# Kernel tuning notes

Hardware: AMD Instinct MI355X
Metric: run time of the kernel (lower is better)

Reference implementation:

```python
import jax, jax.numpy as jnp
import numpy as np

EPS = 1e-5

def _conv1x1(x, W, b):
    # x: [B,Ci,H,W], W: [Co,Ci]
    return jnp.einsum('oi,bihw->bohw', W, x) + b[None, :, None, None]

def _bn(x, gamma, beta, mean, var):
    # inference-mode BatchNorm2d
    s = gamma / jnp.sqrt(var + EPS)
    return x * s[None, :, None, None] + (beta - mean * s)[None, :, None, None]

def _conv3x3(x, W, b):
    y = jax.lax.conv_general_dilated(x, W, (1, 1), 'SAME',
                                     dimension_numbers=('NCHW', 'OIHW', 'NCHW'))
    return y + b[None, :, None, None]

def _sparsemax_last(S):
    # sparsemax over the last axis (TrackHSPA: max-subtract, sort, cumsum, threshold)
    S = S - jnp.max(S, axis=-1, keepdims=True)
    srt = -jnp.sort(-S, axis=-1)                 # descending sort
    csum = jnp.cumsum(srt, axis=-1) - 1.0
    N = S.shape[-1]
    ar = jnp.arange(1, N + 1, dtype=S.dtype)
    mask = ar * srt > csum
    k = jnp.sum(mask, axis=-1, keepdims=True)    # support size per row
    tau = jnp.take_along_axis(csum, k - 1, axis=-1) / k.astype(S.dtype)
    return jnp.maximum(S - tau, 0.0)

def _forward(zf, xf, Wq, bq, Ws, bs, Wg, bg, g_gamma, g_beta, g_mean, g_var,
             Wfi, bfi, fi_gamma, fi_beta, fi_mean, fi_var,
             Wm, bm, m_gamma, m_beta, m_mean, m_var, prelu_a):
    B, C, Hx, Wx = xf.shape
    # ---- Graph_Attention_Union (cross-attention) ----
    xf_t = _conv1x1(xf, Wq, bq).reshape(B, C, -1)      # [B,C,Nx]
    zf_t = _conv1x1(zf, Ws, bs).reshape(B, C, -1)      # [B,C,Nz]
    xf_g = jax.nn.relu(_bn(_conv1x1(xf, Wg, bg), g_gamma, g_beta, g_mean, g_var))
    zf_g = jax.nn.relu(_bn(_conv1x1(zf, Wg, bg), g_gamma, g_beta, g_mean, g_var))
    sim = jnp.einsum('bcn,bcm->bnm', xf_t, zf_t)       # [B,Nx,Nz]
    attn = jax.nn.softmax(sim, axis=2)
    emb = jnp.einsum('bcm,bnm->bcn', zf_g.reshape(B, C, -1), attn)
    emb = emb.reshape(B, C, Hx, Wx)
    gat = jax.nn.relu(_bn(_conv1x1(jnp.concatenate([emb, xf_g], axis=1), Wfi, bfi),
                          fi_gamma, fi_beta, fi_mean, fi_var))
    # ---- TrackHSPA (adaptive sparsemax self-attention) ----
    e = _conv3x3(gat, Wm, bm)
    e = _bn(e, m_gamma, m_beta, m_mean, m_var)
    e = jnp.where(e >= 0, e, prelu_a * e)              # PReLU (single param)
    N = Hx * Wx
    ef = e.reshape(B, -1, N)                           # [B,C',N]
    S = jnp.einsum('bdi,bdj->bij', ef, ef)             # [B,N,N]
    P = _sparsemax_last(S)
    out = jnp.einsum('bcn,bnm->bcm', gat.reshape(B, C, N), P)
    return out.reshape(B, C, Hx, Wx) + gat


def setup_inputs():
    key = jax.random.key(0)
    ks = jax.random.split(key, 8)
    B, C, Hz, Wz, Hx, Wx = 32, 256, 7, 7, 31, 31
    Cm = C // 4
    f = lambda k, shape: jax.random.normal(k, shape, jnp.float32) * 0.05
    return {
        'zf': jax.random.normal(ks[0], (B, C, Hz, Wz), jnp.float32),
        'xf': jax.random.normal(ks[1], (B, C, Hx, Wx), jnp.float32),
        'Wq': f(ks[2], (C, C)), 'bq': jnp.zeros((C,), jnp.float32),
        'Ws': f(ks[3], (C, C)), 'bs': jnp.zeros((C,), jnp.float32),
        'Wg': f(ks[4], (C, C)), 'bg': jnp.zeros((C,), jnp.float32),
        'g_gamma': jnp.ones((C,), jnp.float32), 'g_beta': jnp.zeros((C,), jnp.float32),
        'g_mean': jnp.zeros((C,), jnp.float32), 'g_var': jnp.ones((C,), jnp.float32),
        'Wfi': f(ks[5], (C, 2 * C)), 'bfi': jnp.zeros((C,), jnp.float32),
        'fi_gamma': jnp.ones((C,), jnp.float32), 'fi_beta': jnp.zeros((C,), jnp.float32),
        'fi_mean': jnp.zeros((C,), jnp.float32), 'fi_var': jnp.ones((C,), jnp.float32),
        'Wm': f(ks[6], (Cm, C, 3, 3)), 'bm': jnp.zeros((Cm,), jnp.float32),
        'm_gamma': jnp.ones((Cm,), jnp.float32), 'm_beta': jnp.zeros((Cm,), jnp.float32),
        'm_mean': jnp.zeros((Cm,), jnp.float32), 'm_var': jnp.ones((Cm,), jnp.float32),
        'prelu_a': jnp.array(0.25, jnp.float32),
    }


def reference(zf, xf, Wq, bq, Ws, bs, Wg, bg, g_gamma, g_beta, g_mean, g_var,
              Wfi, bfi, fi_gamma, fi_beta, fi_mean, fi_var,
              Wm, bm, m_gamma, m_beta, m_mean, m_var, prelu_a):
    return _forward(zf, xf, Wq, bq, Ws, bs, Wg, bg, g_gamma, g_beta, g_mean, g_var,
                    Wfi, bfi, fi_gamma, fi_beta, fi_mean, fi_var,
                    Wm, bm, m_gamma, m_beta, m_mean, m_var, prelu_a)
```

## Files before the change

### kernel.cpp

```cpp
#include <hip/hip_runtime.h>
#include <cstdint>
#include <cstddef>
#include <math.h>

typedef __attribute__((ext_vector_type(8))) short short8;
typedef __attribute__((ext_vector_type(4))) float floatx4;
typedef unsigned short ushort_t;

__device__ __forceinline__ ushort_t f2bf(float x) {
    union { float f; unsigned u; } v; v.f = x;
    unsigned r = v.u + 0x7FFF + ((v.u >> 16) & 1);
    return (ushort_t)(r >> 16);
}
__device__ __forceinline__ float bf2f(ushort_t h) {
    union { unsigned u; float f; } v; v.u = ((unsigned)h) << 16; return v.f;
}
__device__ __forceinline__ void split2(float v, ushort_t& h, ushort_t& l) {
    h = f2bf(v);
    l = f2bf(v - bf2f(h));
}

#define MFMA(a, b, c) __builtin_amdgcn_mfma_f32_16x16x32_bf16((a), (b), (c), 0, 0, 0)

__device__ __forceinline__ void gload_lds16(const void* g, void* l) {
    __builtin_amdgcn_global_load_lds(
        (const __attribute__((address_space(1))) unsigned*)g,
        (__attribute__((address_space(3))) unsigned*)l, 16, 0, 0);
}

__global__ void prep_all_kernel(
    const float* __restrict__ Wq, const float* __restrict__ Ws,
    const float* __restrict__ Wg, const float* __restrict__ Wfi,
    const float* __restrict__ Wm,
    const float* bq, const float* bs,
    const float* bg, const float* gg, const float* gb, const float* gm, const float* gv,
    const float* bfi, const float* fg, const float* fb, const float* fm, const float* fv,
    const float* bm, const float* mg, const float* mb, const float* mm, const float* mv,
    ushort_t* Wq_h, ushort_t* Wq_l, ushort_t* Ws_h, ushort_t* Ws_l,
    ushort_t* Wg_h, ushort_t* Wg_l, ushort_t* Wfi_h, ushort_t* Wfi_l,
    ushort_t* wm_h, ushort_t* wm_l, float* scsh)
{
    int bid = blockIdx.x, t = threadIdx.x;
    if (bid < 256) {
        int i = bid * 256 + t; ushort_t h, l; split2(Wq[i], h, l); Wq_h[i] = h; Wq_l[i] = l;
    } else if (bid < 512) {
        int i = (bid - 256) * 256 + t; ushort_t h, l; split2(Ws[i], h, l); Ws_h[i] = h; Ws_l[i] = l;
    } else if (bid < 768) {
        int i = (bid - 512) * 256 + t; ushort_t h, l; split2(Wg[i], h, l); Wg_h[i] = h; Wg_l[i] = l;
    } else if (bid < 1280) {
        int i = (bid - 768) * 256 + t; ushort_t h, l; split2(Wfi[i], h, l); Wfi_h[i] = h; Wfi_l[i] = l;
    } else if (bid < 1856) {
        int i = (bid - 1280) * 256 + t;
        int c = i & 255, m = (i >> 8) & 63, tap = i >> 14;
        ushort_t h, l; split2(Wm[((size_t)m * 256 + c) * 9 + tap], h, l);
        wm_h[i] = h; wm_l[i] = l;
    } else {
        if (t < 256) {
            scsh[t] = 1.f;        scsh[256 + t] = bq[t];
            scsh[512 + t] = 1.f;  scsh[768 + t] = bs[t];
            float s = gg[t] * rsqrtf(gv[t] + 1e-5f);
            scsh[1024 + t] = s;   scsh[1280 + t] = gb[t] + s * (bg[t] - gm[t]);
            float s2 = fg[t] * rsqrtf(fv[t] + 1e-5f);
            scsh[1536 + t] = s2;  scsh[1792 + t] = fb[t] + s2 * (bfi[t] - fm[t]);
            if (t < 64) {
                float s3 = mg[t] * rsqrtf(mv[t] + 1e-5f);
                scsh[2048 + t] = s3; scsh[2112 + t] = mb[t] + s3 * (bm[t] - mm[t]);
            }
        }
    }
}

__global__ void halo_zero_kernel(ushort_t* __restrict__ gxh, ushort_t* __restrict__ gxl) {
    int i = blockIdx.x * 256 + threadIdx.x;
    int b = i >> 7, k = i & 127;
    int r;
    if (k < 33) r = k;
    else if (k < 66) r = 32 * 33 + (k - 33);
    else { int k2 = k - 66; r = ((k2 >> 1) + 1) * 33 + ((k2 & 1) ? 32 : 0); }
    uint4* ph = (uint4*)(gxh + ((size_t)b * 1089 + r) * 256);
    uint4* pl = (uint4*)(gxl + ((size_t)b * 1089 + r) * 256);
    uint4 z = make_uint4(0, 0, 0, 0);
#pragma unroll
    for (int s = 0; s < 32; s++) { ph[s] = z; pl[s] = z; }
}

__global__ __launch_bounds__(256) void transpose_in_kernel(
    const float* __restrict__ in, ushort_t* __restrict__ oh, ushort_t* __restrict__ ol,
    int Nsrc, int Npad)
{
    int b = blockIdx.z;
    const float* ib = in + (size_t)b * 256 * Nsrc;
    ushort_t* obh = oh + (size_t)b * Npad * 256;
    ushort_t* obl = ol + (size_t)b * Npad * 256;
    __shared__ float tile[32][33];
    int n0 = blockIdx.x * 32, c0 = blockIdx.y * 32;
    int tx = threadIdx.x & 31, ty = threadIdx.x >> 5;
#pragma unroll
    for (int r = 0; r < 4; r++) {
        int c = c0 + ty + r * 8, n = n0 + tx;
        tile[ty + r * 8][tx] = (n < Nsrc) ? ib[(size_t)c * Nsrc + n] : 0.f;
    }
    __syncthreads();
#pragma unroll
    for (int r = 0; r < 4; r++) {
        int n = n0 + ty + r * 8, c = c0 + tx;
        if (n < Nsrc) {
            ushort_t h, l; split2(tile[tx][ty + r * 8], h, l);
            obh[(size_t)n * 256 + c] = h;
            obl[(size_t)n * 256 + c] = l;
        }
    }
}

__global__ __launch_bounds__(256, 2) void dualconv_mfma_kernel(
    const ushort_t* __restrict__ Xh, const ushort_t* __restrict__ Xl,
    const ushort_t* __restrict__ W1h, const ushort_t* __restrict__ W1l,
    const ushort_t* __restrict__ W2h, const ushort_t* __restrict__ W2l,
    const float* __restrict__ sc1, const float* __restrict__ sh1,
    const float* __restrict__ sc2, const float* __restrict__ sh2,
    int relu1, int relu2,
    ushort_t* __restrict__ O1h, ushort_t* __restrict__ O1l,
    ushort_t* __restrict__ O2h, ushort_t* __restrict__ O2l,
    ushort_t* __restrict__ O2ch, ushort_t* __restrict__ O2cl, int cpitch,
    int K, int Nvalid, int NpadIn, int NpadOut)
{
    __shared__ ushort_t Bs[32768];
    int b = blockIdx.x;
    int n0 = blockIdx.y * 64;
    const ushort_t* Xbh = Xh + (size_t)b * NpadIn * K;
    const ushort_t* Xbl = Xl + (size_t)b * NpadIn * K;
    int tid = threadIdx.x, w = tid >> 6, l = tid & 63, lc = l & 15, q = l >> 4;
    int m0 = w * 64;

#pragma unroll
    for (int r = 0; r < 16; r++) {
        int d = r * 4096 + w * 1024 + l * 16;
        int dr = d & 32767;
        int row = dr >> 9;
        int inrow = (dr & 511) ^ ((row & 7) << 4);
        int srow = n0 + row; if (srow > NpadIn - 1) srow = NpadIn - 1;
        const ushort_t* src = ((d >> 15) ? Xbl : Xbh) + (size_t)srow * K + (inrow >> 1);
        char* dst = (char*)Bs + (r * 4096 + w * 1024);
        gload_lds16(src, dst);
    }
    __syncthreads();

#define DC_LOADA(K0, AH, AL) do { \
    _Pragma("unroll") \
    for (int mt_ = 0; mt_ < 4; mt_++) { \
        size_t off_ = (size_t)(m0 + mt_ * 16 + lc) * K + (K0) + q * 8; \
        AH[mt_] = *(const short8*)(Wh + off_); \
        AL[mt_] = *(const short8*)(Wl + off_); \
    } \
} while (0)
#define DC_LDSB(K0, BH, BL) do { \
    _Pragma("unroll") \
    for (int jt_ = 0; jt_ < 4; jt_++) { \
        int row_ = jt_ * 16 + lc; \
        int koff_ = (((K0) + q * 8) * 2) ^ ((row_ & 7) << 4); \
        BH[jt_] = *(const short8*)((const char*)Bs + row_ * 512 + koff_); \
        BL[jt_] = *(const short8*)((const char*)Bs + 32768 + row_ * 512 + koff_); \
    } \
} while (0)
#define DC_MFMA(AH, AL, BH, BL) do { \
    _Pragma("unroll") \
    for (int mt_ = 0; mt_ < 4; mt_++) \
    _Pragma("unroll") \
    for (int jt_ = 0; jt_ < 4; jt_++) { \
        acc[mt_][jt_] = MFMA(AH[mt_], BH[jt_], acc[mt_][jt_]); \
        acc[mt_][jt_] = MFMA(AH[mt_], BL[jt_], acc[mt_][jt_]); \
        acc[mt_][jt_] = MFMA(AL[mt_], BH[jt_], acc[mt_][jt_]); \
    } \
} while (0)

    for (int half = 0; half < 2; half++) {
        const ushort_t* Wh = half ? W2h : W1h;
        const ushort_t* Wl = half ? W2l : W1l;
        const float* sc = half ? sc2 : sc1;
        const float* sh = half ? sh2 : sh1;
        int relu = half ? relu2 : relu1;
        ushort_t* Obh = (half ? O2h : O1h) + (size_t)b * NpadOut * 256;
        ushort_t* Obl = (half ? O2l : O1l) + (size_t)b * NpadOut * 256;

        floatx4 acc[4][4];
#pragma unroll
        for (int i = 0; i < 4; i++)
#pragma unroll
            for (int j = 0; j < 4; j++) acc[i][j] = (floatx4){0.f, 0.f, 0.f, 0.f};

        short8 ah0[4], al0[4], ah1[4], al1[4], bh[4], bl[4];
        DC_LOADA(0, ah0, al0);
        for (int k0 = 0; k0 < K; k0 += 64) {
            DC_LOADA(k0 + 32, ah1, al1);
            DC_LDSB(k0, bh, bl);
            DC_MFMA(ah0, al0, bh, bl);
            if (k0 + 64 < K) DC_LOADA(k0 + 64, ah0, al0);
            DC_LDSB(k0 + 32, bh, bl);
            DC_MFMA(ah1, al1, bh, bl);
        }

#pragma unroll
        for (int mt = 0; mt < 4; mt++) {
            int mb = m0 + mt * 16 + q * 4;
            float s0 = sc[mb], s1 = sc[mb + 1], s2 = sc[mb + 2], s3 = sc[mb + 3];
            float h0 = sh[mb], h1 = sh[mb + 1], h2 = sh[mb + 2], h3 = sh[mb + 3];
#pragma unroll
            for (int jt = 0; jt < 4; jt++) {
                int n = n0 + jt * 16 + lc;
                if (n >= Nvalid) continue;
                float v0 = acc[mt][jt][0] * s0 + h0;
                float v1 = acc[mt][jt][1] * s1 + h1;
                float v2 = acc[mt][jt][2] * s2 + h2;
                float v3 = acc[mt][jt][3] * s3 + h3;
                if (relu) { v0 = fmaxf(v0, 0.f); v1 = fmaxf(v1, 0.f); v2 = fmaxf(v2, 0.f); v3 = fmaxf(v3, 0.f); }
                ushort_t e0, f0, e1, f1, e2, f2, e3, f3;
                split2(v0, e0, f0); split2(v1, e1, f1); split2(v2, e2, f2); split2(v3, e3, f3);
                *(ushort4*)(Obh + (size_t)n * 256 + mb) = make_ushort4(e0, e1, e2, e3);
                *(ushort4*)(Obl + (size_t)n * 256 + mb) = make_ushort4(f0, f1, f2, f3);
                if (half && O2ch) {
                    O2ch[((size_t)b * 256 + mb + 0) * cpitch + n] = e0;
                    O2ch[((size_t)b * 256 + mb + 1) * cpitch + n] = e1;
                    O2ch[((size_t)b * 256 + mb + 2) * cpitch + n] = e2;
                    O2ch[((size_t)b * 256 + mb + 3) * cpitch + n] = e3;
                    O2cl[((size_t)b * 256 + mb + 0) * cpitch + n] = f0;
                    O2cl[((size_t)b * 256 + mb + 1) * cpitch + n] = f1;
                    O2cl[((size_t)b * 256 + mb + 2) * cpitch + n] = f2;
                    O2cl[((size_t)b * 256 + mb + 3) * cpitch + n] = f3;
                }
            }
        }
    }
#undef DC_LOADA
#undef DC_LDSB
#undef DC_MFMA
}

__global__ __launch_bounds__(256) void attn_mfma_kernel(
    const ushort_t* __restrict__ xth, const ushort_t* __restrict__ xtl,
    const ushort_t* __restrict__ zth, const ushort_t* __restrict__ ztl,
    const ushort_t* __restrict__ zgh, const ushort_t* __restrict__ zgl,
    ushort_t* __restrict__ eh, ushort_t* __restrict__ el)
{
    __shared__ float S[64][68];
    __shared__ ushort_t awh[64][72], awl[64][72];
    __shared__ float T[4][16][20];
    int b = blockIdx.x, n0 = blockIdx.y * 64;
    int tid = threadIdx.x, w = tid >> 6, l = tid & 63, lc = l & 15, q = l >> 4;
    const ushort_t* xhb = xth + (size_t)b * 992 * 256;
    const ushort_t* xlb = xtl + (size_t)b * 992 * 256;
    const ushort_t* zhb = zth + (size_t)b * 64 * 256;
    const ushort_t* zlb = ztl + (size_t)b * 64 * 256;
    const ushort_t* ghb = zgh + (size_t)b * 256 * 64;
    const ushort_t* glb = zgl + (size_t)b * 256 * 64;

    int rowg = n0 + w * 16 + lc;
#pragma unroll
    for (int ct = 0; ct < 4; ct++) {
        floatx4 acc = (floatx4){0.f, 0.f, 0.f, 0.f};
        for (int k0 = 0; k0 < 256; k0 += 32) {
            short8 ah = *(const short8*)(xhb + (size_t)rowg * 256 + k0 + q * 8);
            short8 al = *(const short8*)(xlb + (size_t)rowg * 256 + k0 + q * 8);
            short8 bh = *(const short8*)(zhb + (size_t)(ct * 16 + lc) * 256 + k0 + q * 8);
            short8 bl = *(const short8*)(zlb + (size_t)(ct * 16 + lc) * 256 + k0 + q * 8);
            acc = MFMA(ah, bh, acc);
            acc = MFMA(ah, bl, acc);
            acc = MFMA(al, bh, acc);
        }
#pragma unroll
        for (int r = 0; r < 4; r++) S[w * 16 + q * 4 + r][ct * 16 + lc] = acc[r];
    }
    __syncthreads();
    if (tid < 64) {
        float mx = -INFINITY;
        for (int m = 0; m < 49; m++) mx = fmaxf(mx, S[tid][m]);
        float sum = 0.f;
        for (int m = 0; m < 49; m++) { float e = __expf(S[tid][m] - mx); S[tid][m] = e; sum += e; }
        float inv = 1.f / sum;
        for (int m = 0; m < 64; m++) {
            float vv = (m < 49) ? S[tid][m] * inv : 0.f;
            ushort_t hh, ll; split2(vv, hh, ll);
            awh[tid][m] = hh; awl[tid][m] = ll;
        }
    }
    __syncthreads();
    int nw = l >> 2, cg = l & 3;
#pragma unroll
    for (int ct = 0; ct < 16; ct++) {
        floatx4 acc = (floatx4){0.f, 0.f, 0.f, 0.f};
#pragma unroll
        for (int k0 = 0; k0 < 64; k0 += 32) {
            short8 ah = *(const short8*)(&awh[w * 16 + lc][k0 + q * 8]);
            short8 al = *(const short8*)(&awl[w * 16 + lc][k0 + q * 8]);
            short8 bh = *(const short8*)(ghb + (size_t)(ct * 16 + lc) * 64 + k0 + q * 8);
            short8 bl = *(const short8*)(glb + (size_t)(ct * 16 + lc) * 64 + k0 + q * 8);
            acc = MFMA(ah, bh, acc);
            acc = MFMA(ah, bl, acc);
            acc = MFMA(al, bh, acc);
        }
#pragma unroll
        for (int r = 0; r < 4; r++) T[w][q * 4 + r][lc] = acc[r];
        float4 vv = *(const float4*)&T[w][nw][cg * 4];
        int n = n0 + w * 16 + nw;
        if (n < 961) {
            ushort_t h0, l0, h1, l1, h2, l2_, h3, l3;
            split2(vv.x, h0, l0); split2(vv.y, h1, l1);
            split2(vv.z, h2, l2_); split2(vv.w, h3, l3);
            size_t off = ((size_t)b * 992 + n) * 256 + ct * 16 + cg * 4;
            *(ushort4*)(eh + off) = make_ushort4(h0, h1, h2, h3);
            *(ushort4*)(el + off) = make_ushort4(l0, l1, l2_, l3);
        }
    }
}

__global__ __launch_bounds__(256, 2) void fi_mfma_kernel(
    const ushort_t* __restrict__ Eh, const ushort_t* __restrict__ El,
    const ushort_t* __restrict__ Gh, const ushort_t* __restrict__ Gl,
    const ushort_t* __restrict__ Wh, const ushort_t* __restrict__ Wl,
    const float* __restrict__ sc, const float* __restrict__ sh,
    ushort_t* __restrict__ gxh, ushort_t* __restrict__ gxl,
    ushort_t* __restrict__ gat_nf)
{
    __shared__ ushort_t Bs[32768];
    int b = blockIdx.x;
    const ushort_t* Ebh = Eh + (size_t)b * 992 * 256;
    const ushort_t* Ebl = El + (size_t)b * 992 * 256;
    const ushort_t* Gbh = Gh + (size_t)b * 992 * 256;
    const ushort_t* Gbl = Gl + (size_t)b * 992 * 256;
    ushort_t* gxhb = gxh + (size_t)b * 1089 * 256;
    ushort_t* gxlb = gxl + (size_t)b * 1089 * 256;
    ushort_t* gn = gat_nf + (size_t)b * 256 * 992;
    int tid = threadIdx.x, w = tid >> 6, l = tid & 63, lc = l & 15, q = l >> 4;
    int m0 = w * 64, nb0 = blockIdx.y * 32;

#pragma unroll
    for (int r = 0; r < 16; r++) {
        int d = r * 4096 + w * 1024 + l * 16;
        int seg = d >> 14;
        int dr = d & 16383;
        int row = dr >> 9;
        int inrow = (dr & 511) ^ ((row & 7) << 4);
        int srow = nb0 + row; if (srow > 991) srow = 991;
        const ushort_t* base = (seg == 0) ? Ebh : (seg == 1) ? Ebl : (seg == 2) ? Gbh : Gbl;
        const ushort_t* src = base + (size_t)srow * 256 + (inrow >> 1);
        char* dst = (char*)Bs + (r * 4096 + w * 1024);
        gload_lds16(src, dst);
    }
    __syncthreads();

    floatx4 acc[4][2];
#pragma unroll
    for (int i = 0; i < 4; i++)
#pragma unroll
        for (int j = 0; j < 2; j++) acc[i][j] = (floatx4){0.f, 0.f, 0.f, 0.f};

#define FI_LOADA(K0, AH, AL) do { \
    _Pragma("unroll") \
    for (int mt_ = 0; mt_ < 4; mt_++) { \
        size_t off_ = (size_t)(m0 + mt_ * 16 + lc) * 512 + (K0) + q * 8; \
        AH[mt_] = *(const short8*)(Wh + off_); \
        AL[mt_] = *(const short8*)(Wl + off_); \
    } \
} while (0)
#define FI_LDSB(K0, BH, BL) do { \
    int segb_ = ((K0) < 256) ? 0 : 32768; \
    int kk_ = (K0) & 255; \
    _Pragma("unroll") \
    for (int jt_ = 0; jt_ < 2; jt_++) { \
        int row_ = jt_ * 16 + lc; \
        int koff_ = ((kk_ + q * 8) * 2) ^ ((row_ & 7) << 4); \
        BH[jt_] = *(const short8*)((const char*)Bs + segb_ + row_ * 512 + koff_); \
        BL[jt_] = *(const short8*)((const char*)Bs + segb_ + 16384 + row_ * 512 + koff_); \
    } \
} while (0)
#define FI_MFMA(AH, AL, BH, BL) do { \
    _Pragma("unroll") \
    for (int mt_ = 0; mt_ < 4; mt_++) \
    _Pragma("unroll") \
    for (int jt_ = 0; jt_ < 2; jt_++) { \
        acc[mt_][jt_] = MFMA(AH[mt_], BH[jt_], acc[mt_][jt_]); \
        acc[mt_][jt_] = MFMA(AH[mt_], BL[jt_], acc[mt_][jt_]); \
        acc[mt_][jt_] = MFMA(AL[mt_], BH[jt_], acc[mt_][jt_]); \
    } \
} while (0)

    {
        short8 ah0[4], al0[4], ah1[4], al1[4], bh[2], bl[2];
        FI_LOADA(0, ah0, al0);
        for (int k0 = 0; k0 < 512; k0 += 64) {
            FI_LOADA(k0 + 32, ah1, al1);
            FI_LDSB(k0, bh, bl);
            FI_MFMA(ah0, al0, bh, bl);
            if (k0 + 64 < 512) FI_LOADA(k0 + 64, ah0, al0);
            FI_LDSB(k0 + 32, bh, bl);
            FI_MFMA(ah1, al1, bh, bl);
        }
    }
#undef FI_LOADA
#undef FI_LDSB
#undef FI_MFMA

#pragma unroll
    for (int mt = 0; mt < 4; mt++) {
        int mb = m0 + mt * 16 + q * 4;
        float s0 = sc[mb], s1 = sc[mb + 1], s2 = sc[mb + 2], s3 = sc[mb + 3];
        float h0 = sh[mb], h1 = sh[mb + 1], h2 = sh[mb + 2], h3 = sh[mb + 3];
#pragma unroll
        for (int jt = 0; jt < 2; jt++) {
            int n = nb0 + jt * 16 + lc;
            if (n >= 961) continue;
            float v0 = fmaxf(acc[mt][jt][0] * s0 + h0, 0.f);
            float v1 = fmaxf(acc[mt][jt][1] * s1 + h1, 0.f);
            float v2 = fmaxf(acc[mt][jt][2] * s2 + h2, 0.f);
            float v3 = fmaxf(acc[mt][jt][3] * s3 + h3, 0.f);
            ushort_t a0, b0, a1, b1, a2, b2, a3, b3;
            split2(v0, a0, b0); split2(v1, a1, b1); split2(v2, a2, b2); split2(v3, a3, b3);
            int hh = n / 31, ww2 = n - hh * 31;
            int row = (hh + 1) * 33 + (ww2 + 1);
            *(ushort4*)(gxhb + (size_t)row * 256 + mb) = make_ushort4(a0, a1, a2, a3);
            *(ushort4*)(gxlb + (size_t)row * 256 + mb) = make_ushort4(b0, b1, b2, b3);
            gn[(size_t)(mb + 0) * 992 + n] = a0;
            gn[(size_t)(mb + 1) * 992 + n] = a1;
            gn[(size_t)(mb + 2) * 992 + n] = a2;
            gn[(size_t)(mb + 3) * 992 + n] = a3;
        }
    }
}

__global__ __launch_bounds__(256, 2) void conv3x3_mfma_kernel(
    const ushort_t* __restrict__ gxh, const ushort_t* __restrict__ gxl,
    const ushort_t* __restrict__ wmh, const ushort_t* __restrict__ wml,
    const float* __restrict__ sc, const float* __restrict__ sh,
    const float* __restrict__ prelu_a,
    ushort_t* __restrict__ eh, ushort_t* __restrict__ el)
{
    __shared__ float Sp[4][2048];
    int b = blockIdx.x;
    const ushort_t* gxhb = gxh + (size_t)b * 1089 * 256;
    const ushort_t* gxlb = gxl + (size_t)b * 1089 * 256;
    ushort_t* ebh = eh + (size_t)b * 1024 * 64;
    ushort_t* ebl = el + (size_t)b * 1024 * 64;
    int tid = threadIdx.x, w = tid >> 6, l = tid & 63, lc = l & 15, q = l >> 4;
    int j0 = blockIdx.y * 64;

    int base[4];
#pragma unroll
    for (int jt = 0; jt < 4; jt++) {
        int j = j0 + jt * 16 + lc; if (j > 960) j = 960;
        int hh = j / 31, ww2 = j - hh * 31;
        base[jt] = (hh + 1) * 33 + (ww2 + 1);
    }

    floatx4 acc[4][4];
#pragma unroll
    for (int i = 0; i < 4; i++)
#pragma unroll
        for (int j = 0; j < 4; j++) acc[i][j] = (floatx4){0.f, 0.f, 0.f, 0.f};

#define C3_LOAD(SL, AH, AL, BH, BL) do { \
    int sl_ = (SL); \
    int tap_ = (sl_ >= 9) ? sl_ - 9 : sl_; \
    int k0_ = (w * 2 + ((sl_ >= 9) ? 1 : 0)) * 32; \
    int doff_ = (tap_ / 3 - 1) * 33 + (tap_ % 3 - 1); \
    const ushort_t* wth_ = wmh + tap_ * 16384; \
    const ushort_t* wtl_ = wml + tap_ * 16384; \
    _Pragma("unroll") \
    for (int mt_ = 0; mt_ < 4; mt_++) { \
        size_t off_ = (size_t)(mt_ * 16 + lc) * 256 + k0_ + q * 8; \
        AH[mt_] = *(const short8*)(wth_ + off_); \
        AL[mt_] = *(const short8*)(wtl_ + off_); \
    } \
    _Pragma("unroll") \
    for (int jt_ = 0; jt_ < 4; jt_++) { \
        size_t off_ = (size_t)(base[jt_] + doff_) * 256 + k0_ + q * 8; \
        BH[jt_] = *(const short8*)(gxhb + off_); \
        BL[jt_] = *(const short8*)(gxlb + off_); \
    } \
} while (0)
#define C3_MFMA(AH, AL, BH, BL) do { \
    _Pragma("unroll") \
    for (int mt_ = 0; mt_ < 4; mt_++) \
    _Pragma("unroll") \
    for (int jt_ = 0; jt_ < 4; jt_++) { \
        acc[mt_][jt_] = MFMA(AH[mt_], BH[jt_], acc[mt_][jt_]); \
        acc[mt_][jt_] = MFMA(AH[mt_], BL[jt_], acc[mt_][jt_]); \
        acc[mt_][jt_] = MFMA(AL[mt_], BH[jt_], acc[mt_][jt_]); \
    } \
} while (0)

    short8 A0h[4], A0l[4], B0h[4], B0l[4];
    short8 A1h[4], A1l[4], B1h[4], B1l[4];
    C3_LOAD(0, A0h, A0l, B0h, B0l);
#pragma unroll
    for (int it = 0; it < 9; it++) {
        C3_LOAD(it * 2 + 1, A1h, A1l, B1h, B1l);
        C3_MFMA(A0h, A0l, B0h, B0l);
        if (it < 8) C3_LOAD(it * 2 + 2, A0h, A0l, B0h, B0l);
        C3_MFMA(A1h, A1l, B1h, B1l);
    }
#undef C3_LOAD
#undef C3_MFMA

    float pa = prelu_a[0];
#pragma unroll
    for (int ph = 0; ph < 2; ph++) {
        __syncthreads();
#pragma unroll
        for (int mt = 0; mt < 4; mt++)
#pragma unroll
            for (int jt = 0; jt < 2; jt++)
#pragma unroll
                for (int r = 0; r < 4; r++)
                    Sp[w][(mt * 16 + q * 4 + r) * 32 + jt * 16 + lc] = acc[mt][ph * 2 + jt][r];
        __syncthreads();
#pragma unroll
        for (int gi = 0; gi < 2; gi++) {
            int g = tid + gi * 256;
            int j = g & 31, mg = g >> 5;
            int m = mg * 4;
            int jj = j0 + ph * 32 + j;
            if (jj >= 961) continue;
            float v[4];
#pragma unroll
            for (int i = 0; i < 4; i++) {
                int idx = (m + i) * 32 + j;
                v[i] = Sp[0][idx] + Sp[1][idx] + Sp[2][idx] + Sp[3][idx];
                v[i] = v[i] * sc[m + i] + sh[m + i];
                v[i] = v[i] >= 0.f ? v[i] : pa * v[i];
            }
            ushort_t a0, b0, a1, b1, a2, b2, a3, b3;
            split2(v[0], a0, b0); split2(v[1], a1, b1);
            split2(v[2], a2, b2); split2(v[3], a3, b3);
            *(ushort4*)(ebh + (size_t)jj * 64 + m) = make_ushort4(a0, a1, a2, a3);
            *(ushort4*)(ebl + (size_t)jj * 64 + m) = make_ushort4(b0, b1, b2, b3);
        }
    }
}

__global__ __launch_bounds__(512) void hspa_mfma_kernel(
    const ushort_t* __restrict__ eh, const ushort_t* __restrict__ el,
    ushort_t* __restrict__ PT)
{
    const int PITCH = 978;
    __shared__ float S[16 * 978];
    int b = blockIdx.x, nb = blockIdx.y;
    const ushort_t* ebh = eh + (size_t)b * 1024 * 64;
    const ushort_t* ebl = el + (size_t)b * 1024 * 64;
    ushort_t* Pb = PT + (size_t)b * 1024 * 992;
    int tid = threadIdx.x, w = tid >> 6, l = tid & 63, lc = l & 15, q = l >> 4;
    int n0 = nb * 16;

    short8 a0h = *(const short8*)(ebh + (size_t)(n0 + lc) * 64 + q * 8);
    short8 a0l = *(const short8*)(ebl + (size_t)(n0 + lc) * 64 + q * 8);
    short8 a1h = *(const short8*)(ebh + (size_t)(n0 + lc) * 64 + 32 + q * 8);
    short8 a1l = *(const short8*)(ebl + (size_t)(n0 + lc) * 64 + 32 + q * 8);

    for (int jt = w; jt < 61; jt += 8) {
        int j = jt * 16 + lc;
        short8 b0h = *(const short8*)(ebh + (size_t)j * 64 + q * 8);
        short8 b0l = *(const short8*)(ebl + (size_t)j * 64 + q * 8);
        short8 b1h = *(const short8*)(ebh + (size_t)j * 64 + 32 + q * 8);
        short8 b1l = *(const short8*)(ebl + (size_t)j * 64 + 32 + q * 8);
        floatx4 acc = (floatx4){0.f, 0.f, 0.f, 0.f};
        acc = MFMA(a0h, b0h, acc);
        acc = MFMA(a0h, b0l, acc);
        acc = MFMA(a0l, b0h, acc);
        acc = MFMA(a1h, b1h, acc);
        acc = MFMA(a1h, b1l, acc);
        acc = MFMA(a1l, b1h, acc);
#pragma unroll
        for (int r = 0; r < 4; r++) S[(q * 4 + r) * PITCH + j] = acc[r];
    }
    __syncthreads();

    int r0 = w * 2, r1 = w * 2 + 1;
    float sv0[16], sv1[16];
    float mx0 = -INFINITY, mx1 = -INFINITY;
#pragma unroll
    for (int t = 0; t < 16; t++) {
        int j = l + t * 64;
        float s0 = (j < 961) ? S[r0 * PITCH + j] : -INFINITY;
        float s1 = (j < 961) ? S[r1 * PITCH + j] : -INFINITY;
        sv0[t] = s0; sv1[t] = s1;
        mx0 = fmaxf(mx0, s0); mx1 = fmaxf(mx1, s1);
    }
    for (int off = 32; off; off >>= 1) {
        mx0 = fmaxf(mx0, __shfl_xor(mx0, off));
        mx1 = fmaxf(mx1, __shfl_xor(mx1, off));
    }
#pragma unroll
    for (int t = 0; t < 16; t++) { sv0[t] -= mx0; sv1[t] -= mx1; }

    float tau0 = -1.f, tau1 = -1.f;
    for (int it = 0; it < 16; it++) {
        float s0 = 0.f, c0 = 0.f, s1 = 0.f, c1 = 0.f;
#pragma unroll
        for (int t = 0; t < 16; t++) {
            if (sv0[t] > tau0) { s0 += sv0[t]; c0 += 1.f; }
            if (sv1[t] > tau1) { s1 += sv1[t]; c1 += 1.f; }
        }
        for (int off = 32; off; off >>= 1) {
            s0 += __shfl_xor(s0, off); c0 += __shfl_xor(c0, off);
            s1 += __shfl_xor(s1, off); c1 += __shfl_xor(c1, off);
        }
        float nt0 = (s0 - 1.f) / c0;
        float nt1 = (s1 - 1.f) / c1;
        bool conv = (nt0 == tau0) && (nt1 == tau1);
        tau0 = nt0; tau1 = nt1;
        if (conv) break;
    }
#pragma unroll
    for (int t = 0; t < 16; t++) {
        int j = l + t * 64;
        if (j < 976) {
            S[r0 * PITCH + j] = (j < 961) ? fmaxf(sv0[t] - tau0, 0.f) : 0.f;
            S[r1 * PITCH + j] = (j < 961) ? fmaxf(sv1[t] - tau1, 0.f) : 0.f;
        }
    }
    __syncthreads();

    for (int j = tid; j < 976; j += 512) {
        union { ushort_t u[8]; uint4 v; } p0, p1;
#pragma unroll
        for (int r = 0; r < 8; r++)  p0.u[r] = f2bf(S[r * PITCH + j]);
#pragma unroll
        for (int r = 0; r < 8; r++)  p1.u[r] = f2bf(S[(8 + r) * PITCH + j]);
        ushort_t* dst = Pb + (size_t)j * 992 + n0;
        *(uint4*)(dst) = p0.v;
        *(uint4*)(dst + 8) = p1.v;
    }
}

__global__ __launch_bounds__(256, 2) void out_mfma_kernel(
    const ushort_t* __restrict__ gat_nf, const ushort_t* __restrict__ PT,
    float* __restrict__ out)
{
    int b = blockIdx.x, jb = blockIdx.y;
    const ushort_t* gb = gat_nf + (size_t)b * 256 * 992;
    const ushort_t* Pb = PT + (size_t)b * 1024 * 992;
    float* ob = out + (size_t)b * 256 * 961;
    int tid = threadIdx.x, w = tid >> 6, l = tid & 63, lc = l & 15, q = l >> 4;
    int m0 = w * 64, j0 = jb * 64;

    floatx4 acc[4][4];
#pragma unroll
    for (int i = 0; i < 4; i++)
#pragma unroll
        for (int j = 0; j < 4; j++) acc[i][j] = (floatx4){0.f, 0.f, 0.f, 0.f};

#define OUT_LOAD(K0, AA, BB) do { \
    _Pragma("unroll") \
    for (int mt_ = 0; mt_ < 4; mt_++) \
        AA[mt_] = *(const short8*)(gb + (size_t)(m0 + mt_ * 16 + lc) * 992 + (K0) + q * 8); \
    _Pragma("unroll") \
    for (int jt_ = 0; jt_ < 4; jt_++) \
        BB[jt_] = *(const short8*)(Pb + (size_t)(j0 + jt_ * 16 + lc) * 992 + (K0) + q * 8); \
} while (0)
#define OUT_MFMA(AA, BB) do { \
    _Pragma("unroll") \
    for (int mt_ = 0; mt_ < 4; mt_++) \
    _Pragma("unroll") \
    for (int jt_ = 0; jt_ < 4; jt_++) \
        acc[mt_][jt_] = MFMA(AA[mt_], BB[jt_], acc[mt_][jt_]); \
} while (0)

    short8 a0[4], b0[4], a1[4], b1[4];
    OUT_LOAD(0, a0, b0);
    for (int k0 = 0; k0 < 960; k0 += 64) {
        OUT_LOAD(k0 + 32, a1, b1);
        OUT_MFMA(a0, b0);
        OUT_LOAD(k0 + 64, a0, b0);
        OUT_MFMA(a1, b1);
    }
    OUT_MFMA(a0, b0);
#undef OUT_LOAD
#undef OUT_MFMA

#pragma unroll
    for (int mt = 0; mt < 4; mt++) {
        int mb = m0 + mt * 16 + q * 4;
#pragma unroll
        for (int jt = 0; jt < 4; jt++) {
            int j = j0 + jt * 16 + lc;
            if (j >= 961) continue;
#pragma unroll
            for (int r = 0; r < 4; r++) {
                float g = bf2f(gb[(size_t)(mb + r) * 992 + j]);
                ob[(size_t)(mb + r) * 961 + j] = acc[mt][jt][r] + g;
            }
        }
    }
}

extern "C" void kernel_launch(void* const* d_in, const int* in_sizes, int n_in,
                              void* d_out, int out_size, void* d_ws, size_t ws_size,
                              hipStream_t stream)
{
    const float* zf      = (const float*)d_in[0];
    const float* xf      = (const float*)d_in[1];
    const float* Wq      = (const float*)d_in[2];
    const float* bq      = (const float*)d_in[3];
    const float* Ws      = (const float*)d_in[4];
    const float* bs      = (const float*)d_in[5];
    const float* Wg      = (const float*)d_in[6];
    const float* bg      = (const float*)d_in[7];
    const float* g_gamma = (const float*)d_in[8];
    const float* g_beta  = (const float*)d_in[9];
    const float* g_mean  = (const float*)d_in[10];
    const float* g_var   = (const float*)d_in[11];
    const float* Wfi     = (const float*)d_in[12];
    const float* bfi     = (const float*)d_in[13];
    const float* fi_gamma= (const float*)d_in[14];
    const float* fi_beta = (const float*)d_in[15];
    const float* fi_mean = (const float*)d_in[16];
    const float* fi_var  = (const float*)d_in[17];
    const float* Wm      = (const float*)d_in[18];
    const float* bm      = (const float*)d_in[19];
    const float* m_gamma = (const float*)d_in[20];
    const float* m_beta  = (const float*)d_in[21];
    const float* m_mean  = (const float*)d_in[22];
    const float* m_var   = (const float*)d_in[23];
    const float* prelu_a = (const float*)d_in[24];
    float* out = (float*)d_out;

    ushort_t* ws = (ushort_t*)d_ws;
    ushort_t* Wq_h  = ws + 0;         ushort_t* Wq_l  = ws + 65536;
    ushort_t* Ws_h  = ws + 131072;    ushort_t* Ws_l  = ws + 196608;
    ushort_t* Wg_h  = ws + 262144;    ushort_t* Wg_l  = ws + 327680;
    ushort_t* Wfi_h = ws + 393216;    ushort_t* Wfi_l = ws + 524288;
    ushort_t* wm_h  = ws + 655360;    ushort_t* wm_l  = ws + 802816;
    ushort_t* XT_h    = ws + 950272;
    ushort_t* XT_l    = ws + 9076736;
    ushort_t* xf_tT_h = ws + 17203200;
    ushort_t* xf_tT_l = ws + 25329664;
    ushort_t* zf_tT_h = ws + 33456128;
    ushort_t* zf_tT_l = ws + 33980416;
    ushort_t* zf_gT_h = ws + 34504704;
    ushort_t* zf_gT_l = ws + 35028992;
    ushort_t* gxT_h   = ws + 17203200;
    ushort_t* gxT_l   = ws + 26124288;
    ushort_t* xf_gT_h = ws + 35553280;
    ushort_t* xf_gT_l = ws + 43679744;
    ushort_t* gat_nf  = ws + 51806208;
    ushort_t* eT_h    = ws + 59932672;
    ushort_t* eT_l    = ws + 62029824;
    ushort_t* PT      = ws + 64126976;
    ushort_t* zfT_h   = ws + 96632832;
    ushort_t* zfT_l   = ws + 97157120;
    float* scsh       = (float*)(ws + 97681408);
    ushort_t* zgC_h   = ws + 97685760;
    ushort_t* zgC_l   = ws + 98210048;
    ushort_t* embT_h = XT_h;
    ushort_t* embT_l = XT_l;

    const float* sc_q  = scsh + 0,    *sh_q  = scsh + 256;
    const float* sc_s  = scsh + 512,  *sh_s  = scsh + 768;
    const float* sc_g  = scsh + 1024, *sh_g  = scsh + 1280;
    const float* sc_fi = scsh + 1536, *sh_fi = scsh + 1792;
    const float* sc_m  = scsh + 2048, *sh_m  = scsh + 2112;

    prep_all_kernel<<<1857, 256, 0, stream>>>(
        Wq, Ws, Wg, Wfi, Wm,
        bq, bs, bg, g_gamma, g_beta, g_mean, g_var,
        bfi, fi_gamma, fi_beta, fi_mean, fi_var,
        bm, m_gamma, m_beta, m_mean, m_var,
        Wq_h, Wq_l, Ws_h, Ws_l, Wg_h, Wg_l, Wfi_h, Wfi_l, wm_h, wm_l, scsh);

    transpose_in_kernel<<<dim3(31, 8, 32), 256, 0, stream>>>(xf, XT_h, XT_l, 961, 992);
    transpose_in_kernel<<<dim3(2, 8, 32), 256, 0, stream>>>(zf, zfT_h, zfT_l, 49, 64);

    dualconv_mfma_kernel<<<dim3(32, 16), 256, 0, stream>>>(
        XT_h, XT_l, Wq_h, Wq_l, Wg_h, Wg_l,
        sc_q, sh_q, sc_g, sh_g, 0, 1,
        xf_tT_h, xf_tT_l, xf_gT_h, xf_gT_l,
        nullptr, nullptr, 0, 256, 961, 992, 992);
    dualconv_mfma_kernel<<<dim3(32, 1), 256, 0, stream>>>(
        zfT_h, zfT_l, Ws_h, Ws_l, Wg_h, Wg_l,
        sc_s, sh_s, sc_g, sh_g, 0, 1,
        zf_tT_h, zf_tT_l, zf_gT_h, zf_gT_l,
        zgC_h, zgC_l, 64, 256, 49, 64, 64);

    attn_mfma_kernel<<<dim3(32, 16), 256, 0, stream>>>(
        xf_tT_h, xf_tT_l, zf_tT_h, zf_tT_l, zgC_h, zgC_l, embT_h, embT_l);

    halo_zero_kernel<<<16, 256, 0, stream>>>(gxT_h, gxT_l);

    fi_mfma_kernel<<<dim3(32, 31), 256, 0, stream>>>(
        embT_h, embT_l, xf_gT_h, xf_gT_l, Wfi_h, Wfi_l, sc_fi, sh_fi,
        gxT_h, gxT_l, gat_nf);

    conv3x3_mfma_kernel<<<dim3(32, 16), 256, 0, stream>>>(
        gxT_h, gxT_l, wm_h, wm_l, sc_m, sh_m, prelu_a, eT_h, eT_l);

    hspa_mfma_kernel<<<dim3(32, 61), 512, 0, stream>>>(eT_h, eT_l, PT);

    out_mfma_kernel<<<dim3(32, 16), 256, 0, stream>>>(gat_nf, PT, out);
}
```

Before: 580.5 us.

## Halve tile sizes and LDS use in dualconv, fi and hspa kernels

Shrinks the dualconv tile from 64 to 32 columns with half the shared memory, and doubles its grid. The fi kernel now stages the E and G operands through one half-size LDS buffer in two passes instead of loading both at once. The hspa kernel processes 8 rows per block instead of 16, with half the shared memory and twice the blocks. The goal is more resident blocks and more parallelism, at the cost of extra A-operand reloads, an added barrier in fi, and idle lanes in hspa, where half the MFMA output rows are discarded.

```diff
diff --git a/kernel.cpp b/kernel.cpp
--- a/kernel.cpp
+++ b/kernel.cpp
@@ -124,22 +124,23 @@
     ushort_t* __restrict__ O2ch, ushort_t* __restrict__ O2cl, int cpitch,
     int K, int Nvalid, int NpadIn, int NpadOut)
 {
-    __shared__ ushort_t Bs[32768];
+    __shared__ ushort_t Bs[16384];
     int b = blockIdx.x;
-    int n0 = blockIdx.y * 64;
+    int n0 = blockIdx.y * 32;
     const ushort_t* Xbh = Xh + (size_t)b * NpadIn * K;
     const ushort_t* Xbl = Xl + (size_t)b * NpadIn * K;
     int tid = threadIdx.x, w = tid >> 6, l = tid & 63, lc = l & 15, q = l >> 4;
     int m0 = w * 64;
 
 #pragma unroll
-    for (int r = 0; r < 16; r++) {
+    for (int r = 0; r < 8; r++) {
         int d = r * 4096 + w * 1024 + l * 16;
-        int dr = d & 32767;
+        int seg = d >> 14;
+        int dr = d & 16383;
         int row = dr >> 9;
         int inrow = (dr & 511) ^ ((row & 7) << 4);
         int srow = n0 + row; if (srow > NpadIn - 1) srow = NpadIn - 1;
-        const ushort_t* src = ((d >> 15) ? Xbl : Xbh) + (size_t)srow * K + (inrow >> 1);
+        const ushort_t* src = (seg ? Xbl : Xbh) + (size_t)srow * K + (inrow >> 1);
         char* dst = (char*)Bs + (r * 4096 + w * 1024);
         gload_lds16(src, dst);
     }
@@ -155,18 +156,18 @@
 } while (0)
 #define DC_LDSB(K0, BH, BL) do { \
     _Pragma("unroll") \
-    for (int jt_ = 0; jt_ < 4; jt_++) { \
+    for (int jt_ = 0; jt_ < 2; jt_++) { \
         int row_ = jt_ * 16 + lc; \
         int koff_ = (((K0) + q * 8) * 2) ^ ((row_ & 7) << 4); \
         BH[jt_] = *(const short8*)((const char*)Bs + row_ * 512 + koff_); \
-        BL[jt_] = *(const short8*)((const char*)Bs + 32768 + row_ * 512 + koff_); \
+        BL[jt_] = *(const short8*)((const char*)Bs + 16384 + row_ * 512 + koff_); \
     } \
 } while (0)
 #define DC_MFMA(AH, AL, BH, BL) do { \
     _Pragma("unroll") \
     for (int mt_ = 0; mt_ < 4; mt_++) \
     _Pragma("unroll") \
-    for (int jt_ = 0; jt_ < 4; jt_++) { \
+    for (int jt_ = 0; jt_ < 2; jt_++) { \
         acc[mt_][jt_] = MFMA(AH[mt_], BH[jt_], acc[mt_][jt_]); \
         acc[mt_][jt_] = MFMA(AH[mt_], BL[jt_], acc[mt_][jt_]); \
         acc[mt_][jt_] = MFMA(AL[mt_], BH[jt_], acc[mt_][jt_]); \
@@ -182,13 +183,13 @@
         ushort_t* Obh = (half ? O2h : O1h) + (size_t)b * NpadOut * 256;
         ushort_t* Obl = (half ? O2l : O1l) + (size_t)b * NpadOut * 256;
 
-        floatx4 acc[4][4];
+        floatx4 acc[4][2];
 #pragma unroll
         for (int i = 0; i < 4; i++)
 #pragma unroll
-            for (int j = 0; j < 4; j++) acc[i][j] = (floatx4){0.f, 0.f, 0.f, 0.f};
-
-        short8 ah0[4], al0[4], ah1[4], al1[4], bh[4], bl[4];
+            for (int j = 0; j < 2; j++) acc[i][j] = (floatx4){0.f, 0.f, 0.f, 0.f};
+
+        short8 ah0[4], al0[4], ah1[4], al1[4], bh[2], bl[2];
         DC_LOADA(0, ah0, al0);
         for (int k0 = 0; k0 < K; k0 += 64) {
             DC_LOADA(k0 + 32, ah1, al1);
@@ -205,7 +206,7 @@
             float s0 = sc[mb], s1 = sc[mb + 1], s2 = sc[mb + 2], s3 = sc[mb + 3];
             float h0 = sh[mb], h1 = sh[mb + 1], h2 = sh[mb + 2], h3 = sh[mb + 3];
 #pragma unroll
-            for (int jt = 0; jt < 4; jt++) {
+            for (int jt = 0; jt < 2; jt++) {
                 int n = n0 + jt * 16 + lc;
                 if (n >= Nvalid) continue;
                 float v0 = acc[mt][jt][0] * s0 + h0;
@@ -320,7 +321,7 @@
     ushort_t* __restrict__ gxh, ushort_t* __restrict__ gxl,
     ushort_t* __restrict__ gat_nf)
 {
-    __shared__ ushort_t Bs[32768];
+    __shared__ ushort_t Bs[16384];
     int b = blockIdx.x;
     const ushort_t* Ebh = Eh + (size_t)b * 992 * 256;
     const ushort_t* Ebl = El + (size_t)b * 992 * 256;
@@ -332,21 +333,6 @@
     int tid = threadIdx.x, w = tid >> 6, l = tid & 63, lc = l & 15, q = l >> 4;
     int m0 = w * 64, nb0 = blockIdx.y * 32;
 
-#pragma unroll
-    for (int r = 0; r < 16; r++) {
-        int d = r * 4096 + w * 1024 + l * 16;
-        int seg = d >> 14;
-        int dr = d & 16383;
-        int row = dr >> 9;
-        int inrow = (dr & 511) ^ ((row & 7) << 4);
-        int srow = nb0 + row; if (srow > 991) srow = 991;
-        const ushort_t* base = (seg == 0) ? Ebh : (seg == 1) ? Ebl : (seg == 2) ? Gbh : Gbl;
-        const ushort_t* src = base + (size_t)srow * 256 + (inrow >> 1);
-        char* dst = (char*)Bs + (r * 4096 + w * 1024);
-        gload_lds16(src, dst);
-    }
-    __syncthreads();
-
     floatx4 acc[4][2];
 #pragma unroll
     for (int i = 0; i < 4; i++)
@@ -362,14 +348,12 @@
     } \
 } while (0)
 #define FI_LDSB(K0, BH, BL) do { \
-    int segb_ = ((K0) < 256) ? 0 : 32768; \
-    int kk_ = (K0) & 255; \
     _Pragma("unroll") \
     for (int jt_ = 0; jt_ < 2; jt_++) { \
         int row_ = jt_ * 16 + lc; \
-        int koff_ = ((kk_ + q * 8) * 2) ^ ((row_ & 7) << 4); \
-        BH[jt_] = *(const short8*)((const char*)Bs + segb_ + row_ * 512 + koff_); \
-        BL[jt_] = *(const short8*)((const char*)Bs + segb_ + 16384 + row_ * 512 + koff_); \
+        int koff_ = (((K0) + q * 8) * 2) ^ ((row_ & 7) << 4); \
+        BH[jt_] = *(const short8*)((const char*)Bs + row_ * 512 + koff_); \
+        BL[jt_] = *(const short8*)((const char*)Bs + 16384 + row_ * 512 + koff_); \
     } \
 } while (0)
 #define FI_MFMA(AH, AL, BH, BL) do { \
@@ -383,15 +367,33 @@
     } \
 } while (0)
 
-    {
+    for (int p = 0; p < 2; p++) {
+        const ushort_t* srcH = p ? Gbh : Ebh;
+        const ushort_t* srcL = p ? Gbl : Ebl;
+        if (p) __syncthreads();
+#pragma unroll
+        for (int r = 0; r < 8; r++) {
+            int d = r * 4096 + w * 1024 + l * 16;
+            int seg = d >> 14;
+            int dr = d & 16383;
+            int row = dr >> 9;
+            int inrow = (dr & 511) ^ ((row & 7) << 4);
+            int srow = nb0 + row; if (srow > 991) srow = 991;
+            const ushort_t* src = (seg ? srcL : srcH) + (size_t)srow * 256 + (inrow >> 1);
+            char* dst = (char*)Bs + (r * 4096 + w * 1024);
+            gload_lds16(src, dst);
+        }
+        __syncthreads();
+
+        int pb = p * 256;
         short8 ah0[4], al0[4], ah1[4], al1[4], bh[2], bl[2];
-        FI_LOADA(0, ah0, al0);
-        for (int k0 = 0; k0 < 512; k0 += 64) {
-            FI_LOADA(k0 + 32, ah1, al1);
-            FI_LDSB(k0, bh, bl);
+        FI_LOADA(pb, ah0, al0);
+        for (int kk = 0; kk < 256; kk += 64) {
+            FI_LOADA(pb + kk + 32, ah1, al1);
+            FI_LDSB(kk, bh, bl);
             FI_MFMA(ah0, al0, bh, bl);
-            if (k0 + 64 < 512) FI_LOADA(k0 + 64, ah0, al0);
-            FI_LDSB(k0 + 32, bh, bl);
+            if (kk + 64 < 256) FI_LOADA(pb + kk + 64, ah0, al0);
+            FI_LDSB(kk + 32, bh, bl);
             FI_MFMA(ah1, al1, bh, bl);
         }
     }
@@ -541,13 +543,13 @@
     ushort_t* __restrict__ PT)
 {
     const int PITCH = 978;
-    __shared__ float S[16 * 978];
+    __shared__ float S[8 * 978];
     int b = blockIdx.x, nb = blockIdx.y;
     const ushort_t* ebh = eh + (size_t)b * 1024 * 64;
     const ushort_t* ebl = el + (size_t)b * 1024 * 64;
     ushort_t* Pb = PT + (size_t)b * 1024 * 992;
     int tid = threadIdx.x, w = tid >> 6, l = tid & 63, lc = l & 15, q = l >> 4;
-    int n0 = nb * 16;
+    int n0 = nb * 8;
 
     short8 a0h = *(const short8*)(ebh + (size_t)(n0 + lc) * 64 + q * 8);
     short8 a0l = *(const short8*)(ebl + (size_t)(n0 + lc) * 64 + q * 8);
@@ -567,66 +569,55 @@
         acc = MFMA(a1h, b1h, acc);
         acc = MFMA(a1h, b1l, acc);
         acc = MFMA(a1l, b1h, acc);
-#pragma unroll
-        for (int r = 0; r < 4; r++) S[(q * 4 + r) * PITCH + j] = acc[r];
+        if (q < 2) {
+#pragma unroll
+            for (int r = 0; r < 4; r++) S[(q * 4 + r) * PITCH + j] = acc[r];
+        }
     }
     __syncthreads();
 
-    int r0 = w * 2, r1 = w * 2 + 1;
-    float sv0[16], sv1[16];
-    float mx0 = -INFINITY, mx1 = -INFINITY;
+    int r0 = w;
+    float sv0[16];
+    float mx0 = -INFINITY;
 #pragma unroll
     for (int t = 0; t < 16; t++) {
         int j = l + t * 64;
         float s0 = (j < 961) ? S[r0 * PITCH + j] : -INFINITY;
-        float s1 = (j < 961) ? S[r1 * PITCH + j] : -INFINITY;
-        sv0[t] = s0; sv1[t] = s1;
-        mx0 = fmaxf(mx0, s0); mx1 = fmaxf(mx1, s1);
-    }
-    for (int off = 32; off; off >>= 1) {
-        mx0 = fmaxf(mx0, __shfl_xor(mx0, off));
-        mx1 = fmaxf(mx1, __shfl_xor(mx1, off));
-    }
-#pragma unroll
-    for (int t = 0; t < 16; t++) { sv0[t] -= mx0; sv1[t] -= mx1; }
-
-    float tau0 = -1.f, tau1 = -1.f;
+        sv0[t] = s0;
+        mx0 = fmaxf(mx0, s0);
+    }
+    for (int off = 32; off; off >>= 1) mx0 = fmaxf(mx0, __shfl_xor(mx0, off));
+#pragma unroll
+    for (int t = 0; t < 16; t++) sv0[t] -= mx0;
+
+    float tau0 = -1.f;
     for (int it = 0; it < 16; it++) {
-        float s0 = 0.f, c0 = 0.f, s1 = 0.f, c1 = 0.f;
+        float s0 = 0.f, c0 = 0.f;
 #pragma unroll
         for (int t = 0; t < 16; t++) {
             if (sv0[t] > tau0) { s0 += sv0[t]; c0 += 1.f; }
-            if (sv1[t] > tau1) { s1 += sv1[t]; c1 += 1.f; }
         }
         for (int off = 32; off; off >>= 1) {
             s0 += __shfl_xor(s0, off); c0 += __shfl_xor(c0, off);
-            s1 += __shfl_xor(s1, off); c1 += __shfl_xor(c1, off);
         }
         float nt0 = (s0 - 1.f) / c0;
-        float nt1 = (s1 - 1.f) / c1;
-        bool conv = (nt0 == tau0) && (nt1 == tau1);
-        tau0 = nt0; tau1 = nt1;
+        bool conv = (nt0 == tau0);
+        tau0 = nt0;
         if (conv) break;
     }
 #pragma unroll
     for (int t = 0; t < 16; t++) {
         int j = l + t * 64;
-        if (j < 976) {
+        if (j < 976)
             S[r0 * PITCH + j] = (j < 961) ? fmaxf(sv0[t] - tau0, 0.f) : 0.f;
-            S[r1 * PITCH + j] = (j < 961) ? fmaxf(sv1[t] - tau1, 0.f) : 0.f;
-        }
     }
     __syncthreads();
 
     for (int j = tid; j < 976; j += 512) {
-        union { ushort_t u[8]; uint4 v; } p0, p1;
+        union { ushort_t u[8]; uint4 v; } p0;
 #pragma unroll
         for (int r = 0; r < 8; r++)  p0.u[r] = f2bf(S[r * PITCH + j]);
-#pragma unroll
-        for (int r = 0; r < 8; r++)  p1.u[r] = f2bf(S[(8 + r) * PITCH + j]);
-        ushort_t* dst = Pb + (size_t)j * 992 + n0;
-        *(uint4*)(dst) = p0.v;
-        *(uint4*)(dst + 8) = p1.v;
+        *(uint4*)(Pb + (size_t)j * 992 + n0) = p0.v;
     }
 }
 
@@ -768,12 +759,12 @@
     transpose_in_kernel<<<dim3(31, 8, 32), 256, 0, stream>>>(xf, XT_h, XT_l, 961, 992);
     transpose_in_kernel<<<dim3(2, 8, 32), 256, 0, stream>>>(zf, zfT_h, zfT_l, 49, 64);
 
-    dualconv_mfma_kernel<<<dim3(32, 16), 256, 0, stream>>>(
+    dualconv_mfma_kernel<<<dim3(32, 31), 256, 0, stream>>>(
         XT_h, XT_l, Wq_h, Wq_l, Wg_h, Wg_l,
         sc_q, sh_q, sc_g, sh_g, 0, 1,
         xf_tT_h, xf_tT_l, xf_gT_h, xf_gT_l,
         nullptr, nullptr, 0, 256, 961, 992, 992);
-    dualconv_mfma_kernel<<<dim3(32, 1), 256, 0, stream>>>(
+    dualconv_mfma_kernel<<<dim3(32, 2), 256, 0, stream>>>(
         zfT_h, zfT_l, Ws_h, Ws_l, Wg_h, Wg_l,
         sc_s, sh_s, sc_g, sh_g, 0, 1,
         zf_tT_h, zf_tT_l, zf_gT_h, zf_gT_l,
@@ -791,7 +782,7 @@
     conv3x3_mfma_kernel<<<dim3(32, 16), 256, 0, stream>>>(
         gxT_h, gxT_l, wm_h, wm_l, sc_m, sh_m, prelu_a, eT_h, eT_l);
 
-    hspa_mfma_kernel<<<dim3(32, 61), 512, 0, stream>>>(eT_h, eT_l, PT);
+    hspa_mfma_kernel<<<dim3(32, 122), 512, 0, stream>>>(eT_h, eT_l, PT);
 
     out_mfma_kernel<<<dim3(32, 16), 256, 0, stream>>>(gat_nf, PT, out);
 }
```

Result: slower. 639.4 us (+10.1%).
